# Kernel optimization log

Measured on AMD Instinct MI355X. Metric: run time of the kernel, lower is better.

## Reference

```python
import jax, jax.numpy as jnp
import numpy as np

DIM = 1024
HEADS = 16


def setup_inputs() -> dict:
    key = jax.random.key(0)
    k1, k2, k3, k4 = jax.random.split(key, 4)
    X = jax.random.normal(k1, (4, 2048, DIM), dtype=jnp.float32)
    # torch Linear weight is [out, in]; store transposed [in, out] for x @ W
    W_qkv = jax.random.normal(k2, (DIM, 3 * DIM), dtype=jnp.float32) * (DIM ** -0.5)
    W_out = jax.random.normal(k3, (DIM, DIM), dtype=jnp.float32) * (DIM ** -0.5)
    b_out = jax.random.normal(k4, (DIM,), dtype=jnp.float32) * 0.01
    return {"X": X, "W_qkv": W_qkv, "W_out": W_out, "b_out": b_out}


def reference(X, W_qkv, W_out, b_out):
    b, t, d = X.shape
    h = HEADS
    hd = d // h
    scale = d ** -0.5  # NOTE: scales by full dim, matching the original module
    qkv = X @ W_qkv  # [b, t, 3d]
    q, k, v = jnp.split(qkv, 3, axis=-1)
    # [b, t, d] -> [b, h, t, hd]
    def to_heads(x):
        return x.reshape(b, t, h, hd).transpose(0, 2, 1, 3)
    q, k, v = to_heads(q), to_heads(k), to_heads(v)
    dots = jnp.einsum('bhid,bhjd->bhij', q, k) * scale  # [b, h, t, t]
    attn = jax.nn.softmax(dots, axis=-1)
    out = jnp.einsum('bhij,bhjd->bhid', attn, v)  # [b, h, t, hd]
    out = out.transpose(0, 2, 1, 3).reshape(b, t, d)
    return out @ W_out + b_out
```

## Files before the change

kernel.cpp:

```cpp
#include <hip/hip_runtime.h>
#include <hip/hip_bf16.h>
#include <stdint.h>

#define DIMD 1024
#define NB 4
#define NT 2048
#define NH 16
#define BT (NB*NT)
#define NQKV (3*DIMD)

typedef __attribute__((ext_vector_type(8))) __bf16 bf16x8;
typedef __attribute__((ext_vector_type(4))) __bf16 bf16x4;
typedef __attribute__((ext_vector_type(4))) float f32x4;
typedef __attribute__((ext_vector_type(16))) float f32x16;

#define MFMA16(a,b,c) __builtin_amdgcn_mfma_f32_16x16x32_bf16((a),(b),(c),0,0,0)
#define MFMA32(a,b,c) __builtin_amdgcn_mfma_f32_32x32x16_bf16((a),(b),(c),0,0,0)

#define QSCALE 0.0450842200277801f

__device__ __forceinline__ void gld16(const void* g, void* l) {
  __builtin_amdgcn_global_load_lds((const __attribute__((address_space(1))) void*)g,
                                   (__attribute__((address_space(3))) void*)l,
                                   16, 0, 0);
}

__device__ __forceinline__ unsigned pkbf(float a, float b) {
  unsigned short ua = __builtin_bit_cast(unsigned short, (__bf16)a);
  unsigned short ub = __builtin_bit_cast(unsigned short, (__bf16)b);
  return (unsigned)ua | ((unsigned)ub << 16);
}

__global__ __launch_bounds__(256) void k_prep(const float* __restrict__ X,
                                              const float* __restrict__ Wqkv,
                                              const float* __restrict__ Wout,
                                              __bf16* __restrict__ Xb,
                                              __bf16* __restrict__ Wqt,
                                              __bf16* __restrict__ Wot) {
  __shared__ __bf16 t[64][72];
  const int bid = blockIdx.x, tid = threadIdx.x;
  if (bid < 1024) {
    const float* in; __bf16* out; int K, N, n0, k0;
    if (bid < 768) { in = Wqkv; out = Wqt; K = 1024; N = 3072; n0 = (bid % 48) * 64; k0 = (bid / 48) * 64; }
    else { int id = bid - 768; in = Wout; out = Wot; K = 1024; N = 1024; n0 = (id % 16) * 64; k0 = (id / 16) * 64; }
    int r = tid >> 2, c0 = (tid & 3) * 16;
    const float4* src = (const float4*)(in + (size_t)(k0 + r) * N + n0 + c0);
#pragma unroll
    for (int i = 0; i < 4; ++i) {
      float4 v = src[i];
      t[r][c0 + i*4 + 0] = (__bf16)v.x;
      t[r][c0 + i*4 + 1] = (__bf16)v.y;
      t[r][c0 + i*4 + 2] = (__bf16)v.z;
      t[r][c0 + i*4 + 3] = (__bf16)v.w;
    }
    __syncthreads();
    bf16x8 o0, o1;
#pragma unroll
    for (int i = 0; i < 8; ++i) o0[i] = t[c0 + i][r];
#pragma unroll
    for (int i = 0; i < 8; ++i) o1[i] = t[c0 + 8 + i][r];
    __bf16* dst = out + (size_t)(n0 + r) * K + k0 + c0;
    *(bf16x8*)dst = o0;
    *(bf16x8*)(dst + 8) = o1;
  } else {
    const int n4 = (BT * DIMD) / 4;
    int i = (bid - 1024) * 256 + tid;
    const int st = 2048 * 256;
    for (; i < n4; i += st) {
      float4 v = ((const float4*)X)[i];
      bf16x4 o;
      o[0] = (__bf16)v.x; o[1] = (__bf16)v.y; o[2] = (__bf16)v.z; o[3] = (__bf16)v.w;
      ((bf16x4*)Xb)[i] = o;
    }
  }
}

template<int MODE>
__global__ __launch_bounds__(256, 3) void k_gemm128(const __bf16* __restrict__ A,
                                                    const __bf16* __restrict__ Bt,
                                                    int nbx,
                                                    __bf16* __restrict__ oQK,
                                                    __bf16* __restrict__ oVt,
                                                    float* __restrict__ oF,
                                                    const float* __restrict__ bias) {
  constexpr int KK = 1024, KT = 32;
  __shared__ alignas(16) char L[3 * 16384];
  const int tid = threadIdx.x;
  const int lane = tid & 63, wid = tid >> 6;
  const int lr = lane & 15, lo = lane >> 4;
  const int wm = wid >> 1, wn = wid & 1;
  const int cpx = gridDim.x >> 3;
  const int swz = (blockIdx.x & 7) * cpx + (blockIdx.x >> 3);
  const int bx = swz % nbx, by = swz / nbx;
  const int m0 = by * 128, n0 = bx * 128;

  const char* gp[4];
  int loff[4];
#pragma unroll
  for (int j = 0; j < 4; ++j) {
    int c = j * 256 + tid;
    int isB = (c >= 512);
    int lc = c & 511;
    int row = lc >> 2, kof = (lc & 3) * 8;
    const __bf16* base = isB ? (Bt + (size_t)(n0 + row) * KK + kof)
                             : (A + (size_t)(m0 + row) * KK + kof);
    gp[j] = (const char*)base;
    loff[j] = c * 16;
  }
  auto STAGE = [&](int s) {
    char* bas = L + s * 16384;
    gld16(gp[0], bas + loff[0]); gp[0] += 64;
    gld16(gp[1], bas + loff[1]); gp[1] += 64;
    gld16(gp[2], bas + loff[2]); gp[2] += 64;
    gld16(gp[3], bas + loff[3]); gp[3] += 64;
  };

  f32x4 acc[4][4] = {};
  STAGE(0); STAGE(1);
  int xs = 2;

  for (int t = 0; t < KT; ++t) {
    if (t == KT - 1) asm volatile("s_waitcnt vmcnt(0)" ::: "memory");
    else             asm volatile("s_waitcnt vmcnt(4)" ::: "memory");
    asm volatile("s_barrier" ::: "memory");
    if (t <= KT - 3) { STAGE(xs); xs = (xs == 2) ? 0 : xs + 1; }
    const __bf16* fa = (const __bf16*)(L + (t % 3) * 16384) + (wm * 64 + lr) * 32 + lo * 8;
    const __bf16* fb = (const __bf16*)(L + (t % 3) * 16384 + 8192) + (wn * 64 + lr) * 32 + lo * 8;
    bf16x8 Af[4], Bf[4];
#pragma unroll
    for (int i = 0; i < 4; ++i) Af[i] = *(const bf16x8*)(fa + i * 512);
#pragma unroll
    for (int j = 0; j < 4; ++j) Bf[j] = *(const bf16x8*)(fb + j * 512);
    __builtin_amdgcn_s_setprio(1);
#pragma unroll
    for (int i = 0; i < 4; ++i)
#pragma unroll
      for (int j = 0; j < 4; ++j)
        acc[i][j] = MFMA16(Af[i], Bf[j], acc[i][j]);
    __builtin_amdgcn_s_setprio(0);
  }

  const int mb = m0 + wm * 64 + lo * 4;
  if (MODE == 0) {
    if (n0 < 1024) {
#pragma unroll
      for (int i = 0; i < 4; ++i)
#pragma unroll
        for (int j = 0; j < 4; ++j) {
          int col = n0 + wn * 64 + j * 16 + lr;
          int row = mb + i * 16;
#pragma unroll
          for (int r = 0; r < 4; ++r)
            oQK[(size_t)(row + r) * 2048 + col] = (__bf16)(acc[i][j][r] * QSCALE);
        }
    } else if (n0 < 2048) {
#pragma unroll
      for (int i = 0; i < 4; ++i)
#pragma unroll
        for (int j = 0; j < 4; ++j) {
          int col = n0 + wn * 64 + j * 16 + lr;
          int row = mb + i * 16;
#pragma unroll
          for (int r = 0; r < 4; ++r)
            oQK[(size_t)(row + r) * 2048 + col] = (__bf16)acc[i][j][r];
        }
    } else {
#pragma unroll
      for (int i = 0; i < 4; ++i)
#pragma unroll
        for (int j = 0; j < 4; ++j) {
          int dd = n0 - 2048 + wn * 64 + j * 16 + lr;
          int row = mb + i * 16;
          int bb = row >> 11, tt = row & 2047;
          bf16x4 pk;
#pragma unroll
          for (int r = 0; r < 4; ++r) pk[r] = (__bf16)acc[i][j][r];
          *(bf16x4*)(oVt + ((size_t)(bb << 10) + dd) * 2048 + tt) = pk;
        }
    }
  } else {
#pragma unroll
    for (int i = 0; i < 4; ++i)
#pragma unroll
      for (int j = 0; j < 4; ++j) {
        int col = n0 + wn * 64 + j * 16 + lr;
        float bv = bias[col];
        int row = mb + i * 16;
#pragma unroll
        for (int r = 0; r < 4; ++r)
          oF[(size_t)(row + r) * 1024 + col] = acc[i][j][r] + bv;
      }
  }
}

__global__ __launch_bounds__(256, 2) void k_attn(const __bf16* __restrict__ QK,
                                                 const __bf16* __restrict__ Vt,
                                                 __bf16* __restrict__ AO) {
  __shared__ alignas(16) char Lsm[3 * 18432];
  const int tid = threadIdx.x, w = tid >> 6, lane = tid & 63;
  const int l31 = lane & 31, hi = lane >> 5;
  const int P = blockIdx.x;
  const int low3 = P & 7, g = P >> 3;
  const int qc = g & 7;
  const int bh = ((g >> 3) << 3) + low3;
  const int h = bh & 15, b = bh >> 4;
  const int q0 = qc * 256 + w * 64;

  bf16x8 qfA[4], qfB[4];
  {
    const __bf16* Qb = QK + (size_t)(b * 2048 + q0 + l31) * 2048 + h * 64 + hi * 8;
#pragma unroll
    for (int dc = 0; dc < 4; ++dc) qfA[dc] = *(const bf16x8*)(Qb + dc * 16);
    Qb += (size_t)32 * 2048;
#pragma unroll
    for (int dc = 0; dc < 4; ++dc) qfB[dc] = *(const bf16x8*)(Qb + dc * 16);
  }
  const __bf16* Kg = QK + (size_t)(b * 2048) * 2048 + 1024 + h * 64;
  const __bf16* Vg = Vt + (size_t)(b * 1024 + h * 64) * 2048;

  const bool nch5 = (tid < 128);
  const char* gp[5];
  int loff[5], advB[5];
#pragma unroll
  for (int j = 0; j < 5; ++j) {
    int c = (j < 4) ? (j * 256 + tid) : (1024 + tid);
    if (c > 1151) c = 1151;
    int isV = (c >= 576);
    int lc = isV ? c - 576 : c;
    int row = lc / 9, col = lc - row * 9; if (col == 8) col = 0;
    const __bf16* gsrc = isV ? (Vg + (size_t)row * 2048 + col * 8)
                             : (Kg + (size_t)row * 2048 + col * 8);
    gp[j] = (const char*)gsrc;
    loff[j] = c * 16;
    advB[j] = isV ? 128 : 262144;
  }

  f32x16 oA0 = {0,0,0,0,0,0,0,0,0,0,0,0,0,0,0,0};
  f32x16 oA1 = {0,0,0,0,0,0,0,0,0,0,0,0,0,0,0,0};
  f32x16 oB0 = {0,0,0,0,0,0,0,0,0,0,0,0,0,0,0,0};
  f32x16 oB1 = {0,0,0,0,0,0,0,0,0,0,0,0,0,0,0,0};
  float lnA = 0.f, lnB = 0.f;

  auto STAGE = [&](int s) {
    char* bas = Lsm + s * 18432;
    gld16(gp[0], bas + loff[0]); gp[0] += advB[0];
    gld16(gp[1], bas + loff[1]); gp[1] += advB[1];
    gld16(gp[2], bas + loff[2]); gp[2] += advB[2];
    gld16(gp[3], bas + loff[3]); gp[3] += advB[3];
    if (nch5) { gld16(gp[4], bas + loff[4]); gp[4] += advB[4]; }
  };

  auto SMPACK = [&](const f32x16& s0, const f32x16& s1, unsigned pw[4][4], float& ln) {
    float p0a[16], p1a[16];
#pragma unroll
    for (int r = 0; r < 16; ++r) {
      p0a[r] = __builtin_amdgcn_exp2f(s0[r]);
      p1a[r] = __builtin_amdgcn_exp2f(s1[r]);
    }
    float sA = 0.f, sB = 0.f, sC = 0.f, sD = 0.f;
#pragma unroll
    for (int r = 0; r < 4; ++r) {
      sA += p0a[r];      sB += p0a[4 + r];
      sC += p0a[8 + r];  sD += p0a[12 + r];
      sA += p1a[r];      sB += p1a[4 + r];
      sC += p1a[8 + r];  sD += p1a[12 + r];
    }
    ln += (sA + sB) + (sC + sD);
#pragma unroll
    for (int c = 0; c < 4; ++c) {
      const float* pp = (c < 2) ? p0a : p1a;
      const int rb = (c & 1) * 8;
      unsigned A01 = pkbf(pp[rb + 0], pp[rb + 1]);
      unsigned A23 = pkbf(pp[rb + 2], pp[rb + 3]);
      unsigned A45 = pkbf(pp[rb + 4], pp[rb + 5]);
      unsigned A67 = pkbf(pp[rb + 6], pp[rb + 7]);
      asm("v_permlane32_swap_b32 %0, %1" : "+v"(A01), "+v"(A45));
      asm("v_permlane32_swap_b32 %0, %1" : "+v"(A23), "+v"(A67));
      pw[c][0] = A01; pw[c][1] = A23; pw[c][2] = A45; pw[c][3] = A67;
    }
  };

  STAGE(0); STAGE(1);
  int xc = 0, xs = 2;

  for (int t = 0; t < 32; ++t) {
    if (t == 31)   asm volatile("s_waitcnt vmcnt(0)" ::: "memory");
    else if (nch5) asm volatile("s_waitcnt vmcnt(5)" ::: "memory");
    else           asm volatile("s_waitcnt vmcnt(4)" ::: "memory");
    __builtin_amdgcn_s_barrier();
    if (t <= 29) { STAGE(xs); xs = (xs == 2) ? 0 : xs + 1; }

    const __bf16* Kl = (const __bf16*)(Lsm + xc * 18432);
    const __bf16* Vl = Kl + 4608;

    f32x16 sA0 = {0,0,0,0,0,0,0,0,0,0,0,0,0,0,0,0};
    f32x16 sA1 = {0,0,0,0,0,0,0,0,0,0,0,0,0,0,0,0};
    f32x16 sB0 = {0,0,0,0,0,0,0,0,0,0,0,0,0,0,0,0};
    f32x16 sB1 = {0,0,0,0,0,0,0,0,0,0,0,0,0,0,0,0};
    {
      bf16x8 kf[8];
#pragma unroll
      for (int dc = 0; dc < 4; ++dc)
        kf[dc] = *(const bf16x8*)(Kl + l31 * 72 + dc * 16 + hi * 8);
#pragma unroll
      for (int dc = 0; dc < 4; ++dc)
        kf[4 + dc] = *(const bf16x8*)(Kl + (32 + l31) * 72 + dc * 16 + hi * 8);
      __builtin_amdgcn_s_setprio(1);
#pragma unroll
      for (int dc = 0; dc < 4; ++dc) {
        sA0 = MFMA32(kf[dc], qfA[dc], sA0);
        sB0 = MFMA32(kf[dc], qfB[dc], sB0);
        sA1 = MFMA32(kf[4 + dc], qfA[dc], sA1);
        sB1 = MFMA32(kf[4 + dc], qfB[dc], sB1);
      }
      __builtin_amdgcn_s_setprio(0);
    }

    unsigned pwA[4][4], pwB[4][4];
    SMPACK(sA0, sA1, pwA, lnA);
    SMPACK(sB0, sB1, pwB, lnB);

    {
      bf16x8 vf[8];
#pragma unroll
      for (int c = 0; c < 4; ++c)
        vf[c] = *(const bf16x8*)(Vl + l31 * 72 + c * 16 + hi * 8);
#pragma unroll
      for (int c = 0; c < 4; ++c)
        vf[4 + c] = *(const bf16x8*)(Vl + (32 + l31) * 72 + c * 16 + hi * 8);
      __builtin_amdgcn_s_setprio(1);
#pragma unroll
      for (int c = 0; c < 4; ++c) {
        union { unsigned u[4]; bf16x8 v; } pa, pb;
        pa.u[0] = pwA[c][0]; pa.u[1] = pwA[c][1]; pa.u[2] = pwA[c][2]; pa.u[3] = pwA[c][3];
        pb.u[0] = pwB[c][0]; pb.u[1] = pwB[c][1]; pb.u[2] = pwB[c][2]; pb.u[3] = pwB[c][3];
        oA0 = MFMA32(pa.v, vf[c], oA0);
        oB0 = MFMA32(pb.v, vf[c], oB0);
        oA1 = MFMA32(pa.v, vf[4 + c], oA1);
        oB1 = MFMA32(pb.v, vf[4 + c], oB1);
      }
      __builtin_amdgcn_s_setprio(0);
    }

    xc = (xc == 2) ? 0 : xc + 1;
  }

  float lA = lnA + __shfl_xor(lnA, 32, 64);
  float lB = lnB + __shfl_xor(lnB, 32, 64);
  float invA = 1.0f / lA, invB = 1.0f / lB;
  __bf16* Ob = AO + (size_t)(b * 2048 + q0) * 1024 + h * 64;
#pragma unroll
  for (int r = 0; r < 16; ++r) {
    int qr = (r & 3) + 8 * (r >> 2) + 4 * hi;
    float ivA = __shfl(invA, qr, 64);
    float ivB = __shfl(invB, qr, 64);
    Ob[(size_t)qr * 1024 + l31] = (__bf16)(oA0[r] * ivA);
    Ob[(size_t)qr * 1024 + 32 + l31] = (__bf16)(oA1[r] * ivA);
    Ob[(size_t)(32 + qr) * 1024 + l31] = (__bf16)(oB0[r] * ivB);
    Ob[(size_t)(32 + qr) * 1024 + 32 + l31] = (__bf16)(oB1[r] * ivB);
  }
}

extern "C" void kernel_launch(void* const* d_in, const int* in_sizes, int n_in,
                              void* d_out, int out_size, void* d_ws, size_t ws_size,
                              hipStream_t stream) {
  const float* X    = (const float*)d_in[0];
  const float* Wqkv = (const float*)d_in[1];
  const float* Wout = (const float*)d_in[2];
  const float* bout = (const float*)d_in[3];
  float* out = (float*)d_out;
  char* ws = (char*)d_ws;

  __bf16* Xb  = (__bf16*)(ws);
  __bf16* Wqt = (__bf16*)(ws + 16777216);
  __bf16* Wot = (__bf16*)(ws + 23068672);
  __bf16* QKb = (__bf16*)(ws + 25165824);
  __bf16* Vtb = (__bf16*)(ws + 58720256);
  __bf16* AOb = (__bf16*)(ws + 75497472);

  k_prep<<<3072, 256, 0, stream>>>(X, Wqkv, Wout, Xb, Wqt, Wot);
  k_gemm128<0><<<1536, 256, 0, stream>>>(Xb, Wqt, 24, QKb, Vtb, nullptr, nullptr);
  k_attn<<<512, 256, 0, stream>>>(QKb, Vtb, AOb);
  k_gemm128<1><<<512, 256, 0, stream>>>(AOb, Wot, 8, nullptr, nullptr, out, bout);
}
```

Baseline: 184.8 us.

## Software-pipeline attention: overlap QK of next tile with PV of previous

Splits the K and V shared-memory staging into separate ring buffers (3 for K, 4 for V) and restructures the loop so that each iteration issues the QK^T MFMAs for tile t and the PV MFMAs for tile t-1 before the softmax of tile t. The aim is to let the exp/pack VALU work overlap with independent matrix-core work and hide the softmax dependency. It uses more LDS (7 buffers of 9216 bytes instead of 3 of 18432), keeps the packed probabilities live across iterations, and makes the wait-count and buffer-index bookkeeping more delicate.

```diff
diff --git a/kernel.cpp b/kernel.cpp
--- a/kernel.cpp
+++ b/kernel.cpp
@@ -196,7 +196,9 @@
 __global__ __launch_bounds__(256, 2) void k_attn(const __bf16* __restrict__ QK,
                                                  const __bf16* __restrict__ Vt,
                                                  __bf16* __restrict__ AO) {
-  __shared__ alignas(16) char Lsm[3 * 18432];
+  __shared__ alignas(16) char Lsm[3 * 9216 + 4 * 9216];
+  char* LsmK = Lsm;
+  char* LsmV = Lsm + 3 * 9216;
   const int tid = threadIdx.x, w = tid >> 6, lane = tid & 63;
   const int l31 = lane & 31, hi = lane >> 5;
   const int P = blockIdx.x;
@@ -218,21 +220,16 @@
   const __bf16* Kg = QK + (size_t)(b * 2048) * 2048 + 1024 + h * 64;
   const __bf16* Vg = Vt + (size_t)(b * 1024 + h * 64) * 2048;
 
-  const bool nch5 = (tid < 128);
-  const char* gp[5];
-  int loff[5], advB[5];
-#pragma unroll
-  for (int j = 0; j < 5; ++j) {
-    int c = (j < 4) ? (j * 256 + tid) : (1024 + tid);
-    if (c > 1151) c = 1151;
-    int isV = (c >= 576);
-    int lc = isV ? c - 576 : c;
+  const char* kgp[3]; int kloff[3];
+  const char* vgp[3]; int vloff[3];
+#pragma unroll
+  for (int j = 0; j < 3; ++j) {
+    int lc = (j < 2) ? (j * 256 + tid) : (512 + (tid & 63));
     int row = lc / 9, col = lc - row * 9; if (col == 8) col = 0;
-    const __bf16* gsrc = isV ? (Vg + (size_t)row * 2048 + col * 8)
-                             : (Kg + (size_t)row * 2048 + col * 8);
-    gp[j] = (const char*)gsrc;
-    loff[j] = c * 16;
-    advB[j] = isV ? 128 : 262144;
+    kgp[j] = (const char*)(Kg + (size_t)row * 2048 + col * 8);
+    vgp[j] = (const char*)(Vg + (size_t)row * 2048 + col * 8);
+    kloff[j] = lc * 16;
+    vloff[j] = lc * 16;
   }
 
   f32x16 oA0 = {0,0,0,0,0,0,0,0,0,0,0,0,0,0,0,0};
@@ -240,14 +237,62 @@
   f32x16 oB0 = {0,0,0,0,0,0,0,0,0,0,0,0,0,0,0,0};
   f32x16 oB1 = {0,0,0,0,0,0,0,0,0,0,0,0,0,0,0,0};
   float lnA = 0.f, lnB = 0.f;
-
-  auto STAGE = [&](int s) {
-    char* bas = Lsm + s * 18432;
-    gld16(gp[0], bas + loff[0]); gp[0] += advB[0];
-    gld16(gp[1], bas + loff[1]); gp[1] += advB[1];
-    gld16(gp[2], bas + loff[2]); gp[2] += advB[2];
-    gld16(gp[3], bas + loff[3]); gp[3] += advB[3];
-    if (nch5) { gld16(gp[4], bas + loff[4]); gp[4] += advB[4]; }
+  unsigned pwA[4][4], pwB[4][4];
+
+  auto STAGE_K = [&](int s) {
+    char* bas = LsmK + s * 9216;
+    gld16(kgp[0], bas + kloff[0]); kgp[0] += 262144;
+    gld16(kgp[1], bas + kloff[1]); kgp[1] += 262144;
+    if (tid < 64) { gld16(kgp[2], bas + kloff[2]); kgp[2] += 262144; }
+  };
+  auto STAGE_V = [&](int s) {
+    char* bas = LsmV + s * 9216;
+    gld16(vgp[0], bas + vloff[0]); vgp[0] += 128;
+    gld16(vgp[1], bas + vloff[1]); vgp[1] += 128;
+    if (tid >= 64 && tid < 128) { gld16(vgp[2], bas + vloff[2]); vgp[2] += 128; }
+  };
+
+  auto QKSTEP = [&](int sK, f32x16& sA0, f32x16& sA1, f32x16& sB0, f32x16& sB1) {
+    const __bf16* Kl = (const __bf16*)(LsmK + sK * 9216);
+    bf16x8 kf[8];
+#pragma unroll
+    for (int dc = 0; dc < 4; ++dc)
+      kf[dc] = *(const bf16x8*)(Kl + l31 * 72 + dc * 16 + hi * 8);
+#pragma unroll
+    for (int dc = 0; dc < 4; ++dc)
+      kf[4 + dc] = *(const bf16x8*)(Kl + (32 + l31) * 72 + dc * 16 + hi * 8);
+    __builtin_amdgcn_s_setprio(1);
+#pragma unroll
+    for (int dc = 0; dc < 4; ++dc) {
+      sA0 = MFMA32(kf[dc], qfA[dc], sA0);
+      sB0 = MFMA32(kf[dc], qfB[dc], sB0);
+      sA1 = MFMA32(kf[4 + dc], qfA[dc], sA1);
+      sB1 = MFMA32(kf[4 + dc], qfB[dc], sB1);
+    }
+    __builtin_amdgcn_s_setprio(0);
+  };
+
+  auto PVSTEP = [&](int sV) {
+    const __bf16* Vl = (const __bf16*)(LsmV + sV * 9216);
+    bf16x8 vf[8];
+#pragma unroll
+    for (int c = 0; c < 4; ++c)
+      vf[c] = *(const bf16x8*)(Vl + l31 * 72 + c * 16 + hi * 8);
+#pragma unroll
+    for (int c = 0; c < 4; ++c)
+      vf[4 + c] = *(const bf16x8*)(Vl + (32 + l31) * 72 + c * 16 + hi * 8);
+    __builtin_amdgcn_s_setprio(1);
+#pragma unroll
+    for (int c = 0; c < 4; ++c) {
+      union { unsigned u[4]; bf16x8 v; } pa, pb;
+      pa.u[0] = pwA[c][0]; pa.u[1] = pwA[c][1]; pa.u[2] = pwA[c][2]; pa.u[3] = pwA[c][3];
+      pb.u[0] = pwB[c][0]; pb.u[1] = pwB[c][1]; pb.u[2] = pwB[c][2]; pb.u[3] = pwB[c][3];
+      oA0 = MFMA32(pa.v, vf[c], oA0);
+      oB0 = MFMA32(pb.v, vf[c], oB0);
+      oA1 = MFMA32(pa.v, vf[4 + c], oA1);
+      oB1 = MFMA32(pb.v, vf[4 + c], oB1);
+    }
+    __builtin_amdgcn_s_setprio(0);
   };
 
   auto SMPACK = [&](const f32x16& s0, const f32x16& s1, unsigned pw[4][4], float& ln) {
@@ -280,70 +325,52 @@
     }
   };
 
-  STAGE(0); STAGE(1);
-  int xc = 0, xs = 2;
-
-  for (int t = 0; t < 32; ++t) {
-    if (t == 31)   asm volatile("s_waitcnt vmcnt(0)" ::: "memory");
-    else if (nch5) asm volatile("s_waitcnt vmcnt(5)" ::: "memory");
-    else           asm volatile("s_waitcnt vmcnt(4)" ::: "memory");
+  const bool five = (tid < 128);
+
+  STAGE_K(0); STAGE_V(0);
+  STAGE_K(1); STAGE_V(1);
+
+  {
+    if (five) asm volatile("s_waitcnt vmcnt(5)" ::: "memory");
+    else      asm volatile("s_waitcnt vmcnt(4)" ::: "memory");
     __builtin_amdgcn_s_barrier();
-    if (t <= 29) { STAGE(xs); xs = (xs == 2) ? 0 : xs + 1; }
-
-    const __bf16* Kl = (const __bf16*)(Lsm + xc * 18432);
-    const __bf16* Vl = Kl + 4608;
-
+    STAGE_K(2); STAGE_V(2);
     f32x16 sA0 = {0,0,0,0,0,0,0,0,0,0,0,0,0,0,0,0};
     f32x16 sA1 = {0,0,0,0,0,0,0,0,0,0,0,0,0,0,0,0};
     f32x16 sB0 = {0,0,0,0,0,0,0,0,0,0,0,0,0,0,0,0};
     f32x16 sB1 = {0,0,0,0,0,0,0,0,0,0,0,0,0,0,0,0};
-    {
-      bf16x8 kf[8];
-#pragma unroll
-      for (int dc = 0; dc < 4; ++dc)
-        kf[dc] = *(const bf16x8*)(Kl + l31 * 72 + dc * 16 + hi * 8);
-#pragma unroll
-      for (int dc = 0; dc < 4; ++dc)
-        kf[4 + dc] = *(const bf16x8*)(Kl + (32 + l31) * 72 + dc * 16 + hi * 8);
-      __builtin_amdgcn_s_setprio(1);
-#pragma unroll
-      for (int dc = 0; dc < 4; ++dc) {
-        sA0 = MFMA32(kf[dc], qfA[dc], sA0);
-        sB0 = MFMA32(kf[dc], qfB[dc], sB0);
-        sA1 = MFMA32(kf[4 + dc], qfA[dc], sA1);
-        sB1 = MFMA32(kf[4 + dc], qfB[dc], sB1);
-      }
-      __builtin_amdgcn_s_setprio(0);
-    }
-
-    unsigned pwA[4][4], pwB[4][4];
+    QKSTEP(0, sA0, sA1, sB0, sB1);
     SMPACK(sA0, sA1, pwA, lnA);
     SMPACK(sB0, sB1, pwB, lnB);
-
-    {
-      bf16x8 vf[8];
-#pragma unroll
-      for (int c = 0; c < 4; ++c)
-        vf[c] = *(const bf16x8*)(Vl + l31 * 72 + c * 16 + hi * 8);
-#pragma unroll
-      for (int c = 0; c < 4; ++c)
-        vf[4 + c] = *(const bf16x8*)(Vl + (32 + l31) * 72 + c * 16 + hi * 8);
-      __builtin_amdgcn_s_setprio(1);
-#pragma unroll
-      for (int c = 0; c < 4; ++c) {
-        union { unsigned u[4]; bf16x8 v; } pa, pb;
-        pa.u[0] = pwA[c][0]; pa.u[1] = pwA[c][1]; pa.u[2] = pwA[c][2]; pa.u[3] = pwA[c][3];
-        pb.u[0] = pwB[c][0]; pb.u[1] = pwB[c][1]; pb.u[2] = pwB[c][2]; pb.u[3] = pwB[c][3];
-        oA0 = MFMA32(pa.v, vf[c], oA0);
-        oB0 = MFMA32(pb.v, vf[c], oB0);
-        oA1 = MFMA32(pa.v, vf[4 + c], oA1);
-        oB1 = MFMA32(pb.v, vf[4 + c], oB1);
-      }
-      __builtin_amdgcn_s_setprio(0);
-    }
-
-    xc = (xc == 2) ? 0 : xc + 1;
-  }
+  }
+
+  int xcK = 1;
+  int xvP = 0;
+  int xsK = 0;
+  int xsV = 3;
+  for (int t = 1; t < 32; ++t) {
+    if (t == 31)   asm volatile("s_waitcnt vmcnt(0)" ::: "memory");
+    else if (five) asm volatile("s_waitcnt vmcnt(5)" ::: "memory");
+    else           asm volatile("s_waitcnt vmcnt(4)" ::: "memory");
+    __builtin_amdgcn_s_barrier();
+    if (t <= 29) { STAGE_K(xsK); STAGE_V(xsV); }
+
+    f32x16 sA0 = {0,0,0,0,0,0,0,0,0,0,0,0,0,0,0,0};
+    f32x16 sA1 = {0,0,0,0,0,0,0,0,0,0,0,0,0,0,0,0};
+    f32x16 sB0 = {0,0,0,0,0,0,0,0,0,0,0,0,0,0,0,0};
+    f32x16 sB1 = {0,0,0,0,0,0,0,0,0,0,0,0,0,0,0,0};
+    QKSTEP(xcK, sA0, sA1, sB0, sB1);
+    PVSTEP(xvP);
+    SMPACK(sA0, sA1, pwA, lnA);
+    SMPACK(sB0, sB1, pwB, lnB);
+
+    xcK = (xcK == 2) ? 0 : xcK + 1;
+    xvP = (xvP == 3) ? 0 : xvP + 1;
+    xsK = (xsK == 2) ? 0 : xsK + 1;
+    xsV = (xsV == 3) ? 0 : xsV + 1;
+  }
+
+  PVSTEP(3);
 
   float lA = lnA + __shfl_xor(lnA, 32, 64);
   float lB = lnB + __shfl_xor(lnB, 32, 64);
```

Result: no change. 188.3 us (+1.9%).

## Split attention KV range across two warp groups per block and reduce via LDS

Applied to the files above, without the earlier changes.

The attention kernel now launches 512 threads per block. Two groups of four waves each process half of the key/value sequence for the same query tile, and their partial outputs and row sums are combined through shared memory at the end. This doubles waves per block to add latency hiding. Each group uses its own double-buffered LDS ring instead of the previous triple buffer with partial waits. It adds a final LDS reduction and synchronisation, and register pressure from launch_bounds(512,4) could cause spills.

```diff
diff --git a/kernel.cpp b/kernel.cpp
--- a/kernel.cpp
+++ b/kernel.cpp
@@ -193,18 +193,20 @@
   }
 }
 
-__global__ __launch_bounds__(256, 2) void k_attn(const __bf16* __restrict__ QK,
+__global__ __launch_bounds__(512, 4) void k_attn(const __bf16* __restrict__ QK,
                                                  const __bf16* __restrict__ Vt,
                                                  __bf16* __restrict__ AO) {
-  __shared__ alignas(16) char Lsm[3 * 18432];
+  __shared__ alignas(16) char Lsm[73728];
   const int tid = threadIdx.x, w = tid >> 6, lane = tid & 63;
+  const int wg = w & 3, g = w >> 2;
+  const int tid_g = tid & 255;
   const int l31 = lane & 31, hi = lane >> 5;
   const int P = blockIdx.x;
-  const int low3 = P & 7, g = P >> 3;
-  const int qc = g & 7;
-  const int bh = ((g >> 3) << 3) + low3;
+  const int low3 = P & 7, gg = P >> 3;
+  const int qc = gg & 7;
+  const int bh = ((gg >> 3) << 3) + low3;
   const int h = bh & 15, b = bh >> 4;
-  const int q0 = qc * 256 + w * 64;
+  const int q0 = qc * 256 + wg * 64;
 
   bf16x8 qfA[4], qfB[4];
   {
@@ -215,15 +217,15 @@
 #pragma unroll
     for (int dc = 0; dc < 4; ++dc) qfB[dc] = *(const bf16x8*)(Qb + dc * 16);
   }
-  const __bf16* Kg = QK + (size_t)(b * 2048) * 2048 + 1024 + h * 64;
-  const __bf16* Vg = Vt + (size_t)(b * 1024 + h * 64) * 2048;
-
-  const bool nch5 = (tid < 128);
+  const __bf16* Kg = QK + (size_t)(b * 2048 + g * 1024) * 2048 + 1024 + h * 64;
+  const __bf16* Vg = Vt + (size_t)(b * 1024 + h * 64) * 2048 + g * 1024;
+
+  const bool nch5 = (tid_g < 128);
   const char* gp[5];
   int loff[5], advB[5];
 #pragma unroll
   for (int j = 0; j < 5; ++j) {
-    int c = (j < 4) ? (j * 256 + tid) : (1024 + tid);
+    int c = (j < 4) ? (j * 256 + tid_g) : (1024 + tid_g);
     if (c > 1151) c = 1151;
     int isV = (c >= 576);
     int lc = isV ? c - 576 : c;
@@ -235,6 +237,8 @@
     advB[j] = isV ? 128 : 262144;
   }
 
+  char* ring = Lsm + g * 36864;
+
   f32x16 oA0 = {0,0,0,0,0,0,0,0,0,0,0,0,0,0,0,0};
   f32x16 oA1 = {0,0,0,0,0,0,0,0,0,0,0,0,0,0,0,0};
   f32x16 oB0 = {0,0,0,0,0,0,0,0,0,0,0,0,0,0,0,0};
@@ -242,7 +246,7 @@
   float lnA = 0.f, lnB = 0.f;
 
   auto STAGE = [&](int s) {
-    char* bas = Lsm + s * 18432;
+    char* bas = ring + s * 18432;
     gld16(gp[0], bas + loff[0]); gp[0] += advB[0];
     gld16(gp[1], bas + loff[1]); gp[1] += advB[1];
     gld16(gp[2], bas + loff[2]); gp[2] += advB[2];
@@ -280,17 +284,14 @@
     }
   };
 
-  STAGE(0); STAGE(1);
-  int xc = 0, xs = 2;
-
-  for (int t = 0; t < 32; ++t) {
-    if (t == 31)   asm volatile("s_waitcnt vmcnt(0)" ::: "memory");
-    else if (nch5) asm volatile("s_waitcnt vmcnt(5)" ::: "memory");
-    else           asm volatile("s_waitcnt vmcnt(4)" ::: "memory");
+  STAGE(0);
+
+  for (int t = 0; t < 16; ++t) {
+    asm volatile("s_waitcnt vmcnt(0)" ::: "memory");
     __builtin_amdgcn_s_barrier();
-    if (t <= 29) { STAGE(xs); xs = (xs == 2) ? 0 : xs + 1; }
-
-    const __bf16* Kl = (const __bf16*)(Lsm + xc * 18432);
+    if (t < 15) STAGE((t + 1) & 1);
+
+    const __bf16* Kl = (const __bf16*)(ring + (t & 1) * 18432);
     const __bf16* Vl = Kl + 4608;
 
     f32x16 sA0 = {0,0,0,0,0,0,0,0,0,0,0,0,0,0,0,0};
@@ -341,23 +342,57 @@
       }
       __builtin_amdgcn_s_setprio(0);
     }
-
-    xc = (xc == 2) ? 0 : xc + 1;
   }
 
   float lA = lnA + __shfl_xor(lnA, 32, 64);
   float lB = lnB + __shfl_xor(lnB, 32, 64);
-  float invA = 1.0f / lA, invB = 1.0f / lB;
-  __bf16* Ob = AO + (size_t)(b * 2048 + q0) * 1024 + h * 64;
-#pragma unroll
-  for (int r = 0; r < 16; ++r) {
-    int qr = (r & 3) + 8 * (r >> 2) + 4 * hi;
-    float ivA = __shfl(invA, qr, 64);
-    float ivB = __shfl(invB, qr, 64);
-    Ob[(size_t)qr * 1024 + l31] = (__bf16)(oA0[r] * ivA);
-    Ob[(size_t)qr * 1024 + 32 + l31] = (__bf16)(oA1[r] * ivA);
-    Ob[(size_t)(32 + qr) * 1024 + l31] = (__bf16)(oB0[r] * ivB);
-    Ob[(size_t)(32 + qr) * 1024 + 32 + l31] = (__bf16)(oB1[r] * ivB);
+
+  __syncthreads();
+  f32x4* qbase = (f32x4*)(Lsm + wg * 16384);
+  float* lnp = (float*)(Lsm + 65536) + (size_t)(wg * 64 + lane) * 2;
+  if (g == 1) {
+#pragma unroll
+    for (int i = 0; i < 4; ++i) {
+      f32x4 q0v = {oA0[i*4+0], oA0[i*4+1], oA0[i*4+2], oA0[i*4+3]};
+      f32x4 q1v = {oA1[i*4+0], oA1[i*4+1], oA1[i*4+2], oA1[i*4+3]};
+      f32x4 q2v = {oB0[i*4+0], oB0[i*4+1], oB0[i*4+2], oB0[i*4+3]};
+      f32x4 q3v = {oB1[i*4+0], oB1[i*4+1], oB1[i*4+2], oB1[i*4+3]};
+      qbase[(0 + i) * 64 + lane] = q0v;
+      qbase[(4 + i) * 64 + lane] = q1v;
+      qbase[(8 + i) * 64 + lane] = q2v;
+      qbase[(12 + i) * 64 + lane] = q3v;
+    }
+    lnp[0] = lA; lnp[1] = lB;
+  }
+  __syncthreads();
+  if (g == 0) {
+#pragma unroll
+    for (int i = 0; i < 4; ++i) {
+      f32x4 q0v = qbase[(0 + i) * 64 + lane];
+      f32x4 q1v = qbase[(4 + i) * 64 + lane];
+      f32x4 q2v = qbase[(8 + i) * 64 + lane];
+      f32x4 q3v = qbase[(12 + i) * 64 + lane];
+#pragma unroll
+      for (int r = 0; r < 4; ++r) {
+        oA0[i*4+r] += q0v[r];
+        oA1[i*4+r] += q1v[r];
+        oB0[i*4+r] += q2v[r];
+        oB1[i*4+r] += q3v[r];
+      }
+    }
+    lA += lnp[0]; lB += lnp[1];
+    float invA = 1.0f / lA, invB = 1.0f / lB;
+    __bf16* Ob = AO + (size_t)(b * 2048 + q0) * 1024 + h * 64;
+#pragma unroll
+    for (int r = 0; r < 16; ++r) {
+      int qr = (r & 3) + 8 * (r >> 2) + 4 * hi;
+      float ivA = __shfl(invA, qr, 64);
+      float ivB = __shfl(invB, qr, 64);
+      Ob[(size_t)qr * 1024 + l31] = (__bf16)(oA0[r] * ivA);
+      Ob[(size_t)qr * 1024 + 32 + l31] = (__bf16)(oA1[r] * ivA);
+      Ob[(size_t)(32 + qr) * 1024 + l31] = (__bf16)(oB0[r] * ivB);
+      Ob[(size_t)(32 + qr) * 1024 + 32 + l31] = (__bf16)(oB1[r] * ivB);
+    }
   }
 }
 
@@ -380,6 +415,6 @@
 
   k_prep<<<3072, 256, 0, stream>>>(X, Wqkv, Wout, Xb, Wqt, Wot);
   k_gemm128<0><<<1536, 256, 0, stream>>>(Xb, Wqt, 24, QKb, Vtb, nullptr, nullptr);
-  k_attn<<<512, 256, 0, stream>>>(QKb, Vtb, AOb);
+  k_attn<<<512, 512, 0, stream>>>(QKb, Vtb, AOb);
   k_gemm128<1><<<512, 256, 0, stream>>>(AOb, Wot, 8, nullptr, nullptr, out, bout);
 }
```

Result: slower. 617.4 us (+234.1%).
